# Kernel tuning notes

Measured on AMD Instinct MI355X. Metric: run time of the kernel, lower is better.

The kernel has to match this reference:

```python
import jax, jax.numpy as jnp
import numpy as np

N_NODES = 100000
N_EDGES = 3200000
HID = 16


def _graph_conv(x, src, dst, w_rel, w_root, b_rel, num_nodes):
    # PyG GraphConv: out_i = lin_rel(sum_{j in N(i)} x_j) + lin_root(x_i)
    agg = jax.ops.segment_sum(x[src], dst, num_segments=num_nodes)  # [N, d_in]
    return agg @ w_rel + b_rel + x @ w_root


def setup_inputs() -> dict:
    key = jax.random.key(0)
    ks = jax.random.split(key, 8)
    x = jax.random.normal(ks[0], (N_NODES, 1), dtype=jnp.float32)
    edge_index = jax.random.randint(ks[1], (2, N_EDGES), 0, N_NODES, dtype=jnp.int64)
    s = 1.0 / np.sqrt(HID)
    return {
        "x": x,
        "edge_index": edge_index,
        "enc_w_rel": jax.random.uniform(ks[2], (1, HID), jnp.float32, -1.0, 1.0),
        "enc_w_root": jax.random.uniform(ks[3], (1, HID), jnp.float32, -1.0, 1.0),
        "enc_b": jnp.zeros((HID,), jnp.float32),
        "proc_w_rel": jax.random.uniform(ks[4], (HID, HID), jnp.float32, -s, s),
        "proc_w_root": jax.random.uniform(ks[5], (HID, HID), jnp.float32, -s, s),
        "proc_b": jnp.zeros((HID,), jnp.float32),
        "dec_w_rel": jax.random.uniform(ks[6], (HID, 1), jnp.float32, -s, s),
        "dec_w_root": jax.random.uniform(ks[7], (HID, 1), jnp.float32, -s, s),
        "dec_b": jnp.zeros((1,), jnp.float32),
    }


def reference(x, edge_index, enc_w_rel, enc_w_root, enc_b,
              proc_w_rel, proc_w_root, proc_b,
              dec_w_rel, dec_w_root, dec_b):
    num_nodes = x.shape[0]
    src, dst = edge_index[0], edge_index[1]
    z = _graph_conv(x, src, dst, enc_w_rel, enc_w_root, enc_b, num_nodes)
    z = jax.nn.relu(z)
    z = _graph_conv(z, src, dst, proc_w_rel, proc_w_root, proc_b, num_nodes)
    y = _graph_conv(z, src, dst, dec_w_rel, dec_w_root, dec_b, num_nodes)
    return jax.nn.relu(y)
```

## Files before the change

kernel.cpp:

```cpp
#include <hip/hip_runtime.h>
#include <hip/hip_bf16.h>

#define HID 16
#define SB_BITS 11
#define SBLK (1 << SB_BITS)
#define SUBS 128
#define NBMAX 64
#define GSTRIDE 16
#define PT_THREADS 512
#define PT_K 8
#define PT_EDGES (PT_THREADS * PT_K)
#define ROWP 65

__global__ void k_init(int* __restrict__ p, int n) {
    int i = blockIdx.x * blockDim.x + threadIdx.x;
    if (i < n) p[i] = 0;
}

__global__ void __launch_bounds__(PT_THREADS)
k_passA(const int* __restrict__ src, const int* __restrict__ dst,
        unsigned* __restrict__ bucketsA, int* __restrict__ gcurA,
        int E, int nb, int capA) {
    __shared__ int cnt[NBMAX];
    __shared__ int pos[NBMAX];
    __shared__ int gbase[NBMAX];
    __shared__ unsigned reorder[PT_EDGES];
    __shared__ unsigned char bbk[PT_EDGES];
    int tb = blockIdx.x * PT_EDGES;
    int nE = min(PT_EDGES, E - tb);
    if (threadIdx.x < nb) cnt[threadIdx.x] = 0;
    __syncthreads();
    int kk[PT_K]; int rk[PT_K]; unsigned pk[PT_K];
    int ebase = tb + threadIdx.x * PT_K;
    if (ebase + PT_K <= E) {
        uint4 s0 = *(const uint4*)(src + ebase);
        uint4 s1 = *(const uint4*)(src + ebase + 4);
        uint4 d0 = *(const uint4*)(dst + ebase);
        uint4 d1 = *(const uint4*)(dst + ebase + 4);
        int ss[PT_K] = {(int)s0.x,(int)s0.y,(int)s0.z,(int)s0.w,
                        (int)s1.x,(int)s1.y,(int)s1.z,(int)s1.w};
        int dd[PT_K] = {(int)d0.x,(int)d0.y,(int)d0.z,(int)d0.w,
                        (int)d1.x,(int)d1.y,(int)d1.z,(int)d1.w};
#pragma unroll
        for (int k = 0; k < PT_K; k++) {
            int b = dd[k] >> SB_BITS;
            kk[k] = b;
            pk[k] = ((unsigned)(dd[k] & (SBLK - 1)) << 17) | (unsigned)ss[k];
            rk[k] = atomicAdd(&cnt[b], 1);
        }
    } else {
#pragma unroll
        for (int k = 0; k < PT_K; k++) {
            int e = ebase + k;
            if (e < E) {
                int s = src[e], d = dst[e];
                int b = d >> SB_BITS;
                kk[k] = b;
                pk[k] = ((unsigned)(d & (SBLK - 1)) << 17) | (unsigned)s;
                rk[k] = atomicAdd(&cnt[b], 1);
            } else kk[k] = -1;
        }
    }
    __syncthreads();
    if (threadIdx.x == 0) {
        int acc = 0;
        for (int b = 0; b < nb; b++) { pos[b] = acc; acc += cnt[b]; }
    }
    __syncthreads();
    if (threadIdx.x < nb && cnt[threadIdx.x] > 0)
        gbase[threadIdx.x] = atomicAdd(&gcurA[threadIdx.x * GSTRIDE], cnt[threadIdx.x]);
    __syncthreads();
#pragma unroll
    for (int k = 0; k < PT_K; k++) {
        if (kk[k] >= 0) {
            int idx = pos[kk[k]] + rk[k];
            reorder[idx] = pk[k];
            bbk[idx] = (unsigned char)kk[k];
        }
    }
    __syncthreads();
    for (int idx = threadIdx.x; idx < nE; idx += PT_THREADS) {
        int b = bbk[idx];
        int g = gbase[b] + (idx - pos[b]);
        if (g < capA) bucketsA[(size_t)b * capA + g] = reorder[idx];
    }
}

__global__ void __launch_bounds__(PT_THREADS)
k_passB(const unsigned* __restrict__ bucketsA, const int* __restrict__ gcurA,
        unsigned* __restrict__ bucketsB, int* __restrict__ gcurB,
        int capA, int capSub, int tilesB) {
    int j = blockIdx.x / tilesB;
    int tile = blockIdx.x - j * tilesB;
    int cnt_j = min(gcurA[j * GSTRIDE], capA);
    int tb = tile * PT_EDGES;
    if (tb >= cnt_j) return;
    int nE = min(PT_EDGES, cnt_j - tb);
    __shared__ int cnt[SUBS];
    __shared__ int pos[SUBS];
    __shared__ int gb[SUBS];
    __shared__ unsigned reorder[PT_EDGES];
    if (threadIdx.x < SUBS) cnt[threadIdx.x] = 0;
    __syncthreads();
    const unsigned* in = bucketsA + (size_t)j * capA + tb;
    int kk[PT_K]; int rk[PT_K]; unsigned pk[PT_K];
    int ebase = threadIdx.x * PT_K;
    if (ebase + PT_K <= nE) {
        uint4 p0 = *(const uint4*)(in + ebase);
        uint4 p1 = *(const uint4*)(in + ebase + 4);
        unsigned pp[PT_K] = {p0.x, p0.y, p0.z, p0.w, p1.x, p1.y, p1.z, p1.w};
#pragma unroll
        for (int k = 0; k < PT_K; k++) {
            int s = (int)(pp[k] >> 21);
            kk[k] = s;
            pk[k] = pp[k];
            rk[k] = atomicAdd(&cnt[s], 1);
        }
    } else {
#pragma unroll
        for (int k = 0; k < PT_K; k++) {
            int e = ebase + k;
            if (e < nE) {
                unsigned p = in[e];
                int s = (int)(p >> 21);
                kk[k] = s;
                pk[k] = p;
                rk[k] = atomicAdd(&cnt[s], 1);
            } else kk[k] = -1;
        }
    }
    __syncthreads();
    if (threadIdx.x == 0) {
        int acc = 0;
        for (int s = 0; s < SUBS; s++) { pos[s] = acc; acc += cnt[s]; }
    }
    __syncthreads();
    if (threadIdx.x < SUBS && cnt[threadIdx.x] > 0)
        gb[threadIdx.x] = atomicAdd(&gcurB[j * SUBS + threadIdx.x], cnt[threadIdx.x]);
    __syncthreads();
#pragma unroll
    for (int k = 0; k < PT_K; k++) {
        if (kk[k] >= 0) {
            int idx = pos[kk[k]] + rk[k];
            reorder[idx] = pk[k];
        }
    }
    __syncthreads();
    for (int idx = threadIdx.x; idx < nE; idx += PT_THREADS) {
        unsigned p = reorder[idx];
        int s = (int)(p >> 21);
        unsigned outp = ((p & 0x1FFFFu) << 4) | ((p >> 17) & 15u);
        int g = gb[s] + (idx - pos[s]);
        if (g < capSub) bucketsB[(size_t)(j * SUBS + s) * capSub + g] = outp;
    }
}

__global__ void __launch_bounds__(256)
k_agg1enc(const unsigned* __restrict__ bk2, const int* __restrict__ gcurB,
          const float* __restrict__ x,
          const float* __restrict__ ewrel, const float* __restrict__ ewroot,
          const float* __restrict__ eb,
          const float* __restrict__ pwrel, const float* __restrict__ pwroot,
          const float* __restrict__ dwrel, const float* __restrict__ dwroot,
          float* __restrict__ SAB, float* __restrict__ G1, float* __restrict__ G2,
          int capSub, int N) {
    __shared__ float P[4 * 16 * ROWP];
    __shared__ float su1[HID], su2[HID], sv1[HID], sv2[HID];
    __shared__ float swr[HID], swo[HID], sbb[HID];
    int t = threadIdx.x;
    if (t < 64) {
        int k = t & 15, w = t >> 4;
        const float* M  = (w < 2) ? pwrel : pwroot;
        const float* vv = ((w & 1) == 0) ? dwrel : dwroot;
        float acc = 0.f;
        for (int h = 0; h < HID; h++) acc += M[k * HID + h] * vv[h];
        if (w == 0) su1[k] = acc;
        else if (w == 1) su2[k] = acc;
        else if (w == 2) sv1[k] = acc;
        else sv2[k] = acc;
    }
    if (t < HID) { swr[t] = ewrel[t]; swo[t] = ewroot[t]; sbb[t] = eb[t]; }
    int wv = t >> 6, lane = t & 63;
    int q = blockIdx.x * 4 + wv;
    float* p = P + wv * 16 * ROWP;
#pragma unroll
    for (int d = 0; d < 16; d++) p[d * ROWP + lane] = 0.f;
    __syncthreads();
    int cnt = min(gcurB[q], capSub);
    const unsigned* bk = bk2 + (size_t)q * capSub;
    int base = 0;
    for (; base + 256 <= cnt; base += 256) {
        uint4 p4 = *(const uint4*)(bk + base + (lane << 2));
        float v0 = x[p4.x >> 4], v1 = x[p4.y >> 4], v2 = x[p4.z >> 4], v3 = x[p4.w >> 4];
        p[(int)(p4.x & 15) * ROWP + lane] += v0;
        p[(int)(p4.y & 15) * ROWP + lane] += v1;
        p[(int)(p4.z & 15) * ROWP + lane] += v2;
        p[(int)(p4.w & 15) * ROWP + lane] += v3;
    }
    for (int e = base + lane; e < cnt; e += 64) {
        unsigned pk = bk[e];
        p[(int)(pk & 15) * ROWP + lane] += x[pk >> 4];
    }
    __builtin_amdgcn_wave_barrier();
    int d = lane & 15, c0 = (lane >> 4) * 16;
    float s = 0.f;
#pragma unroll
    for (int k = 0; k < 16; k++) s += p[d * ROWP + c0 + k];
    s += __shfl_xor(s, 16);
    s += __shfl_xor(s, 32);
    if (lane < 16) {
        int n = q * 16 + lane;
        if (n < N) {
            float a1 = s, xi = x[n];
            float sa = 0.f, sb = 0.f, g1 = 0.f, g2 = 0.f;
#pragma unroll
            for (int h = 0; h < HID; h++) {
                float z = fmaxf(fmaf(a1, swr[h], fmaf(xi, swo[h], sbb[h])), 0.f);
                sa = fmaf(z, su1[h], sa);
                sb = fmaf(z, su2[h], sb);
                g1 = fmaf(z, sv1[h], g1);
                g2 = fmaf(z, sv2[h], g2);
            }
            ((float2*)SAB)[n] = make_float2(sa, sb);
            G1[n] = g1; G2[n] = g2;
        }
    }
}

__global__ void __launch_bounds__(256)
k_agg2mid(const unsigned* __restrict__ bk2, const int* __restrict__ gcurB,
          const float* __restrict__ SAB,
          const float* __restrict__ G1, const float* __restrict__ G2,
          const float* __restrict__ pb, const float* __restrict__ dwrel,
          const float* __restrict__ dwroot, const float* __restrict__ db,
          float* __restrict__ BETA, float* __restrict__ R,
          int capSub, int N) {
    __shared__ float2 P2[4 * 16 * ROWP];
    __shared__ float sc1, sc2, sbd;
    int t = threadIdx.x;
    if (t == 0) {
        float c1 = 0.f, c2 = 0.f;
        for (int h = 0; h < HID; h++) { c1 += pb[h] * dwrel[h]; c2 += pb[h] * dwroot[h]; }
        sc1 = c1; sc2 = c2; sbd = db[0];
    }
    int wv = t >> 6, lane = t & 63;
    int q = blockIdx.x * 4 + wv;
    float2* pw = P2 + wv * 16 * ROWP;
#pragma unroll
    for (int d = 0; d < 16; d++) pw[d * ROWP + lane] = make_float2(0.f, 0.f);
    __syncthreads();
    int cnt = min(gcurB[q], capSub);
    const unsigned* bk = bk2 + (size_t)q * capSub;
    const float2* v2 = (const float2*)SAB;
    int base = 0;
    for (; base + 256 <= cnt; base += 256) {
        uint4 p4 = *(const uint4*)(bk + base + (lane << 2));
        float2 v0 = v2[p4.x >> 4], v1 = v2[p4.y >> 4];
        float2 w2 = v2[p4.z >> 4], w3 = v2[p4.w >> 4];
        float2* s0 = &pw[(int)(p4.x & 15) * ROWP + lane];
        s0->x += v0.x; s0->y += v0.y;
        float2* s1 = &pw[(int)(p4.y & 15) * ROWP + lane];
        s1->x += v1.x; s1->y += v1.y;
        float2* s2 = &pw[(int)(p4.z & 15) * ROWP + lane];
        s2->x += w2.x; s2->y += w2.y;
        float2* s3 = &pw[(int)(p4.w & 15) * ROWP + lane];
        s3->x += w3.x; s3->y += w3.y;
    }
    for (int e = base + lane; e < cnt; e += 64) {
        unsigned pk = bk[e];
        float2 v = v2[pk >> 4];
        float2* s = &pw[(int)(pk & 15) * ROWP + lane];
        s->x += v.x; s->y += v.y;
    }
    __builtin_amdgcn_wave_barrier();
    int d = lane & 15, c0 = (lane >> 4) * 16;
    float sa = 0.f, sb = 0.f;
#pragma unroll
    for (int k = 0; k < 16; k++) {
        float2 v = pw[d * ROWP + c0 + k];
        sa += v.x; sb += v.y;
    }
    sa += __shfl_xor(sa, 16); sa += __shfl_xor(sa, 32);
    sb += __shfl_xor(sb, 16); sb += __shfl_xor(sb, 32);
    if (lane < 16) {
        int n = q * 16 + lane;
        if (n < N) {
            BETA[n] = sa + G1[n] + sc1;
            R[n]    = sb + G2[n] + sc2 + sbd;
        }
    }
}

__global__ void __launch_bounds__(256)
k_agg1f(const unsigned* __restrict__ bk2, const int* __restrict__ gcurB,
        const float* __restrict__ val, const float* __restrict__ R,
        float* __restrict__ out, int capSub, int N) {
    __shared__ float P[4 * 16 * ROWP];
    int wv = threadIdx.x >> 6, lane = threadIdx.x & 63;
    int q = blockIdx.x * 4 + wv;
    float* p = P + wv * 16 * ROWP;
#pragma unroll
    for (int d = 0; d < 16; d++) p[d * ROWP + lane] = 0.f;
    int cnt = min(gcurB[q], capSub);
    const unsigned* bk = bk2 + (size_t)q * capSub;
    int base = 0;
    for (; base + 256 <= cnt; base += 256) {
        uint4 p4 = *(const uint4*)(bk + base + (lane << 2));
        float v0 = val[p4.x >> 4], v1 = val[p4.y >> 4];
        float v2 = val[p4.z >> 4], v3 = val[p4.w >> 4];
        p[(int)(p4.x & 15) * ROWP + lane] += v0;
        p[(int)(p4.y & 15) * ROWP + lane] += v1;
        p[(int)(p4.z & 15) * ROWP + lane] += v2;
        p[(int)(p4.w & 15) * ROWP + lane] += v3;
    }
    for (int e = base + lane; e < cnt; e += 64) {
        unsigned pk = bk[e];
        p[(int)(pk & 15) * ROWP + lane] += val[pk >> 4];
    }
    __builtin_amdgcn_wave_barrier();
    int d = lane & 15, c0 = (lane >> 4) * 16;
    float s = 0.f;
#pragma unroll
    for (int k = 0; k < 16; k++) s += p[d * ROWP + c0 + k];
    s += __shfl_xor(s, 16);
    s += __shfl_xor(s, 32);
    if (lane < 16) {
        int n = q * 16 + lane;
        if (n < N) out[n] = fmaxf(s + R[n], 0.f);
    }
}

extern "C" void kernel_launch(void* const* d_in, const int* in_sizes, int n_in,
                              void* d_out, int out_size, void* d_ws, size_t ws_size,
                              hipStream_t stream) {
    const float* x      = (const float*)d_in[0];
    const int*   ei     = (const int*)d_in[1];
    const float* ewrel  = (const float*)d_in[2];
    const float* ewroot = (const float*)d_in[3];
    const float* eb     = (const float*)d_in[4];
    const float* pwrel  = (const float*)d_in[5];
    const float* pwroot = (const float*)d_in[6];
    const float* pb     = (const float*)d_in[7];
    const float* dwrel  = (const float*)d_in[8];
    const float* dwroot = (const float*)d_in[9];
    const float* db     = (const float*)d_in[10];
    float* out = (float*)d_out;

    const int N = in_sizes[0];
    const int E = in_sizes[1] / 2;
    const int* src = ei;
    const int* dst = ei + E;

    const int nb = (N + SBLK - 1) >> SB_BITS;
    int capA = ((E / nb + 2048) + PT_EDGES - 1) & ~(PT_EDGES - 1);
    const int tilesB = capA / PT_EDGES;
    const int nq = nb * SUBS;
    int capSub = ((E / nq + 226) + 3) & ~3;

    size_t off = 0;
    int* gcurA = (int*)d_ws;                    off += NBMAX * GSTRIDE;
    int* gcurB = (int*)d_ws + off;              off += nq;
    const int zeroWords = (int)off;
    off = (off + 255) & ~(size_t)255;
    unsigned* bucketsA = (unsigned*)d_ws + off; off += (size_t)nb * capA;
    unsigned* bucketsB = (unsigned*)d_ws + off; off += (size_t)nq * capSub;
    float* SAB  = (float*)d_ws + off;           off += (size_t)2 * N;
    float* G1   = (float*)d_ws + off;           off += N;
    float* G2   = (float*)d_ws + off;           off += N;
    float* BETA = (float*)d_ws + off;           off += N;
    float* R    = (float*)d_ws + off;           off += N;

    const int ntilesA = (E + PT_EDGES - 1) / PT_EDGES;
    const int aggBlocks = nq / 4;

    hipLaunchKernelGGL(k_init, dim3((zeroWords + 255) / 256), dim3(256), 0, stream,
                       gcurA, zeroWords);
    hipLaunchKernelGGL(k_passA, dim3(ntilesA), dim3(PT_THREADS), 0, stream,
                       src, dst, bucketsA, gcurA, E, nb, capA);
    hipLaunchKernelGGL(k_passB, dim3(nb * tilesB), dim3(PT_THREADS), 0, stream,
                       bucketsA, gcurA, bucketsB, gcurB, capA, capSub, tilesB);

    hipLaunchKernelGGL(k_agg1enc, dim3(aggBlocks), dim3(256), 0, stream,
                       bucketsB, gcurB, x, ewrel, ewroot, eb, pwrel, pwroot,
                       dwrel, dwroot, SAB, G1, G2, capSub, N);
    hipLaunchKernelGGL(k_agg2mid, dim3(aggBlocks), dim3(256), 0, stream,
                       bucketsB, gcurB, SAB, G1, G2, pb, dwrel, dwroot, db,
                       BETA, R, capSub, N);
    hipLaunchKernelGGL(k_agg1f, dim3(aggBlocks), dim3(256), 0, stream,
                       bucketsB, gcurB, BETA, R, out, capSub, N);
}
```

Before: 174.2 us.

## Prefetch x gather into bucket pass and widen aggregation loops to eight edges

The second bucketing pass now gathers x[src] for each edge and writes it into a parallel value array next to the packed bucket entries. The first aggregation then reads those values contiguously instead of doing a random gather into x. All three aggregation kernels also handle eight edges per lane per iteration instead of four, so more gather loads are in flight at once. The cost is an extra E-sized float array written and read back, a larger shared-memory footprint in passB, and a longer scalar tail loop when bucket sizes are not multiples of 512.

```diff
diff --git a/kernel.cpp b/kernel.cpp
--- a/kernel.cpp
+++ b/kernel.cpp
@@ -1,5 +1,4 @@
 #include <hip/hip_runtime.h>
-#include <hip/hip_bf16.h>
 
 #define HID 16
 #define SB_BITS 11
@@ -88,7 +87,9 @@
 
 __global__ void __launch_bounds__(PT_THREADS)
 k_passB(const unsigned* __restrict__ bucketsA, const int* __restrict__ gcurA,
-        unsigned* __restrict__ bucketsB, int* __restrict__ gcurB,
+        const float* __restrict__ x,
+        unsigned* __restrict__ bucketsB, float* __restrict__ xvB,
+        int* __restrict__ gcurB,
         int capA, int capSub, int tilesB) {
     int j = blockIdx.x / tilesB;
     int tile = blockIdx.x - j * tilesB;
@@ -100,15 +101,18 @@
     __shared__ int pos[SUBS];
     __shared__ int gb[SUBS];
     __shared__ unsigned reorder[PT_EDGES];
+    __shared__ float reorderv[PT_EDGES];
     if (threadIdx.x < SUBS) cnt[threadIdx.x] = 0;
     __syncthreads();
     const unsigned* in = bucketsA + (size_t)j * capA + tb;
-    int kk[PT_K]; int rk[PT_K]; unsigned pk[PT_K];
+    int kk[PT_K]; int rk[PT_K]; unsigned pk[PT_K]; float xv[PT_K];
     int ebase = threadIdx.x * PT_K;
     if (ebase + PT_K <= nE) {
         uint4 p0 = *(const uint4*)(in + ebase);
         uint4 p1 = *(const uint4*)(in + ebase + 4);
         unsigned pp[PT_K] = {p0.x, p0.y, p0.z, p0.w, p1.x, p1.y, p1.z, p1.w};
+#pragma unroll
+        for (int k = 0; k < PT_K; k++) xv[k] = x[pp[k] & 0x1FFFFu];
 #pragma unroll
         for (int k = 0; k < PT_K; k++) {
             int s = (int)(pp[k] >> 21);
@@ -125,6 +129,7 @@
                 int s = (int)(p >> 21);
                 kk[k] = s;
                 pk[k] = p;
+                xv[k] = x[p & 0x1FFFFu];
                 rk[k] = atomicAdd(&cnt[s], 1);
             } else kk[k] = -1;
         }
@@ -143,20 +148,27 @@
         if (kk[k] >= 0) {
             int idx = pos[kk[k]] + rk[k];
             reorder[idx] = pk[k];
+            reorderv[idx] = xv[k];
         }
     }
     __syncthreads();
     for (int idx = threadIdx.x; idx < nE; idx += PT_THREADS) {
         unsigned p = reorder[idx];
+        float v = reorderv[idx];
         int s = (int)(p >> 21);
         unsigned outp = ((p & 0x1FFFFu) << 4) | ((p >> 17) & 15u);
         int g = gb[s] + (idx - pos[s]);
-        if (g < capSub) bucketsB[(size_t)(j * SUBS + s) * capSub + g] = outp;
+        if (g < capSub) {
+            size_t o = (size_t)(j * SUBS + s) * capSub + g;
+            bucketsB[o] = outp;
+            xvB[o] = v;
+        }
     }
 }
 
 __global__ void __launch_bounds__(256)
-k_agg1enc(const unsigned* __restrict__ bk2, const int* __restrict__ gcurB,
+k_agg1enc(const unsigned* __restrict__ bk2, const float* __restrict__ xvB,
+          const int* __restrict__ gcurB,
           const float* __restrict__ x,
           const float* __restrict__ ewrel, const float* __restrict__ ewroot,
           const float* __restrict__ eb,
@@ -188,18 +200,24 @@
     __syncthreads();
     int cnt = min(gcurB[q], capSub);
     const unsigned* bk = bk2 + (size_t)q * capSub;
+    const float* xq = xvB + (size_t)q * capSub;
     int base = 0;
-    for (; base + 256 <= cnt; base += 256) {
-        uint4 p4 = *(const uint4*)(bk + base + (lane << 2));
-        float v0 = x[p4.x >> 4], v1 = x[p4.y >> 4], v2 = x[p4.z >> 4], v3 = x[p4.w >> 4];
-        p[(int)(p4.x & 15) * ROWP + lane] += v0;
-        p[(int)(p4.y & 15) * ROWP + lane] += v1;
-        p[(int)(p4.z & 15) * ROWP + lane] += v2;
-        p[(int)(p4.w & 15) * ROWP + lane] += v3;
+    for (; base + 512 <= cnt; base += 512) {
+        const unsigned* bp = bk + base + (lane << 3);
+        const float* vp = xq + base + (lane << 3);
+        uint4 a4 = *(const uint4*)bp;
+        uint4 b4 = *(const uint4*)(bp + 4);
+        float4 va = *(const float4*)vp;
+        float4 vb = *(const float4*)(vp + 4);
+        unsigned pp[8] = {a4.x, a4.y, a4.z, a4.w, b4.x, b4.y, b4.z, b4.w};
+        float vv[8] = {va.x, va.y, va.z, va.w, vb.x, vb.y, vb.z, vb.w};
+#pragma unroll
+        for (int k = 0; k < 8; k++)
+            p[(int)(pp[k] & 15) * ROWP + lane] += vv[k];
     }
     for (int e = base + lane; e < cnt; e += 64) {
         unsigned pk = bk[e];
-        p[(int)(pk & 15) * ROWP + lane] += x[pk >> 4];
+        p[(int)(pk & 15) * ROWP + lane] += xq[e];
     }
     __builtin_amdgcn_wave_barrier();
     int d = lane & 15, c0 = (lane >> 4) * 16;
@@ -253,18 +271,19 @@
     const unsigned* bk = bk2 + (size_t)q * capSub;
     const float2* v2 = (const float2*)SAB;
     int base = 0;
-    for (; base + 256 <= cnt; base += 256) {
-        uint4 p4 = *(const uint4*)(bk + base + (lane << 2));
-        float2 v0 = v2[p4.x >> 4], v1 = v2[p4.y >> 4];
-        float2 w2 = v2[p4.z >> 4], w3 = v2[p4.w >> 4];
-        float2* s0 = &pw[(int)(p4.x & 15) * ROWP + lane];
-        s0->x += v0.x; s0->y += v0.y;
-        float2* s1 = &pw[(int)(p4.y & 15) * ROWP + lane];
-        s1->x += v1.x; s1->y += v1.y;
-        float2* s2 = &pw[(int)(p4.z & 15) * ROWP + lane];
-        s2->x += w2.x; s2->y += w2.y;
-        float2* s3 = &pw[(int)(p4.w & 15) * ROWP + lane];
-        s3->x += w3.x; s3->y += w3.y;
+    for (; base + 512 <= cnt; base += 512) {
+        const unsigned* bp = bk + base + (lane << 3);
+        uint4 a4 = *(const uint4*)bp;
+        uint4 b4 = *(const uint4*)(bp + 4);
+        unsigned pp[8] = {a4.x, a4.y, a4.z, a4.w, b4.x, b4.y, b4.z, b4.w};
+        float2 vv[8];
+#pragma unroll
+        for (int k = 0; k < 8; k++) vv[k] = v2[pp[k] >> 4];
+#pragma unroll
+        for (int k = 0; k < 8; k++) {
+            float2* s = &pw[(int)(pp[k] & 15) * ROWP + lane];
+            s->x += vv[k].x; s->y += vv[k].y;
+        }
     }
     for (int e = base + lane; e < cnt; e += 64) {
         unsigned pk = bk[e];
@@ -304,14 +323,17 @@
     int cnt = min(gcurB[q], capSub);
     const unsigned* bk = bk2 + (size_t)q * capSub;
     int base = 0;
-    for (; base + 256 <= cnt; base += 256) {
-        uint4 p4 = *(const uint4*)(bk + base + (lane << 2));
-        float v0 = val[p4.x >> 4], v1 = val[p4.y >> 4];
-        float v2 = val[p4.z >> 4], v3 = val[p4.w >> 4];
-        p[(int)(p4.x & 15) * ROWP + lane] += v0;
-        p[(int)(p4.y & 15) * ROWP + lane] += v1;
-        p[(int)(p4.z & 15) * ROWP + lane] += v2;
-        p[(int)(p4.w & 15) * ROWP + lane] += v3;
+    for (; base + 512 <= cnt; base += 512) {
+        const unsigned* bp = bk + base + (lane << 3);
+        uint4 a4 = *(const uint4*)bp;
+        uint4 b4 = *(const uint4*)(bp + 4);
+        unsigned pp[8] = {a4.x, a4.y, a4.z, a4.w, b4.x, b4.y, b4.z, b4.w};
+        float vv[8];
+#pragma unroll
+        for (int k = 0; k < 8; k++) vv[k] = val[pp[k] >> 4];
+#pragma unroll
+        for (int k = 0; k < 8; k++)
+            p[(int)(pp[k] & 15) * ROWP + lane] += vv[k];
     }
     for (int e = base + lane; e < cnt; e += 64) {
         unsigned pk = bk[e];
@@ -364,6 +386,7 @@
     off = (off + 255) & ~(size_t)255;
     unsigned* bucketsA = (unsigned*)d_ws + off; off += (size_t)nb * capA;
     unsigned* bucketsB = (unsigned*)d_ws + off; off += (size_t)nq * capSub;
+    float* xvB  = (float*)d_ws + off;           off += (size_t)nq * capSub;
     float* SAB  = (float*)d_ws + off;           off += (size_t)2 * N;
     float* G1   = (float*)d_ws + off;           off += N;
     float* G2   = (float*)d_ws + off;           off += N;
@@ -378,10 +401,10 @@
     hipLaunchKernelGGL(k_passA, dim3(ntilesA), dim3(PT_THREADS), 0, stream,
                        src, dst, bucketsA, gcurA, E, nb, capA);
     hipLaunchKernelGGL(k_passB, dim3(nb * tilesB), dim3(PT_THREADS), 0, stream,
-                       bucketsA, gcurA, bucketsB, gcurB, capA, capSub, tilesB);
+                       bucketsA, gcurA, x, bucketsB, xvB, gcurB, capA, capSub, tilesB);
 
     hipLaunchKernelGGL(k_agg1enc, dim3(aggBlocks), dim3(256), 0, stream,
-                       bucketsB, gcurB, x, ewrel, ewroot, eb, pwrel, pwroot,
+                       bucketsB, xvB, gcurB, x, ewrel, ewroot, eb, pwrel, pwroot,
                        dwrel, dwroot, SAB, G1, G2, capSub, N);
     hipLaunchKernelGGL(k_agg2mid, dim3(aggBlocks), dim3(256), 0, stream,
                        bucketsB, gcurB, SAB, G1, G2, pb, dwrel, dwroot, db,
```

Measured after the change: 178.1 us. 1.02x slower.
